# Performance work log

Hardware: AMD Instinct MI355X
Metric: run time of the kernel (lower is better)

Reference implementation:

```python
import jax, jax.numpy as jnp
import numpy as np

B, S, D = 4, 2048, 256   # batch, seq, d_output (= d_k = d_v here)
H = 8                    # num_head


def setup_inputs() -> dict:
    key = jax.random.key(0)
    ks = jax.random.split(key, 8)
    Q = jax.random.normal(ks[0], (B, S, D), dtype=jnp.float32)
    K = jax.random.normal(ks[1], (B, S, D), dtype=jnp.float32)
    V = jax.random.normal(ks[2], (B, S, D), dtype=jnp.float32)
    M = jax.random.uniform(ks[3], (B, S, S), dtype=jnp.float32)  # multiplicative mask
    # per-head projection weights, stacked over heads (truncated_normal ~ normal here)
    W_Q = jax.random.normal(ks[4], (H, D, D), dtype=jnp.float32) * 0.05
    W_K = jax.random.normal(ks[5], (H, D, D), dtype=jnp.float32) * 0.05
    W_V = jax.random.normal(ks[6], (H, D, D), dtype=jnp.float32) * 0.05
    W_mh = jax.random.normal(ks[7], (H * D, D), dtype=jnp.float32) * 0.05
    return {"Q": Q, "K": K, "V": V, "M": M,
            "W_Q": W_Q, "W_K": W_K, "W_V": W_V, "W_mh": W_mh}


def reference(Q, K, V, M, W_Q, W_K, W_V, W_mh):
    d_k = W_Q.shape[-1]
    scale = 1.0 / np.sqrt(d_k).astype(np.float32)
    # per-head projections, vectorized over heads
    Qh = jnp.einsum('bsd,hdk->bhsk', Q, W_Q)          # [B,H,S,dk]
    Kh = jnp.einsum('bsd,hdk->bhsk', K, W_K)          # [B,H,S,dk]
    Vh = jnp.einsum('bsd,hdv->bhsv', V, W_V)          # [B,H,S,dv]
    # scaled similarity with MULTIPLICATIVE mask applied before softmax
    scores = jnp.einsum('bhsk,bhtk->bhst', Qh, Kh) * scale * M[:, None]
    attn = jax.nn.softmax(scores, axis=-1)            # [B,H,S,S]
    heads = jnp.einsum('bhst,bhtv->bhsv', attn, Vh)   # [B,H,S,dv]
    # concat heads along feature dim: [B,S,H*dv]
    Bv, Hv, Sv, Dv = heads.shape
    heads = heads.transpose(0, 2, 1, 3).reshape(Bv, Sv, Hv * Dv)
    return heads @ W_mh                               # [B,S,d_output]
```

## Files before the change

### kernel.cpp

```cpp
#include <hip/hip_runtime.h>
#include <hip/hip_bf16.h>
#include <stdint.h>

#define B_ 4
#define S_ 2048
#define D_ 256
#define H_ 8

using f32x4  = __attribute__((ext_vector_type(4))) float;
using bf16x8 = __attribute__((ext_vector_type(8))) __bf16;

static __device__ __forceinline__ unsigned short f2bf(float x) {
    union { float f; unsigned u; } v; v.f = x;
    unsigned r = (v.u + 0x7FFFu + ((v.u >> 16) & 1u)) >> 16;
    return (unsigned short)r;
}

static __device__ __forceinline__ f32x4 mfma_bf16(bf16x8 a, bf16x8 b, f32x4 c) {
    return __builtin_amdgcn_mfma_f32_16x16x32_bf16(a, b, c, 0, 0, 0);
}

__global__ __launch_bounds__(256) void wtrans_kernel(
        const float* __restrict__ Wq, const float* __restrict__ Wk,
        const float* __restrict__ Wv, const float* __restrict__ Wmh,
        unsigned short* __restrict__ WqkvT, unsigned short* __restrict__ WmhT) {
    int idx = blockIdx.x * 256 + threadIdx.x;
    const int NQKV = 3 * H_ * 256 * 256;
    if (idx < NQKV) {
        int d = idx & 255, n = (idx >> 8) & 255, h = (idx >> 16) & 7, which = idx >> 19;
        const float* W = (which == 0) ? Wq : ((which == 1) ? Wk : Wv);
        WqkvT[idx] = f2bf(W[(h * 256 + d) * 256 + n]);
    } else {
        int j = idx - NQKV;
        int k = j & 2047, n = j >> 11;
        WmhT[j] = f2bf(Wmh[k * 256 + n]);
    }
}

__global__ __launch_bounds__(256, 2) void proj_kernel(
        const float* __restrict__ Q, const float* __restrict__ K,
        const float* __restrict__ V, const unsigned short* __restrict__ WqkvT,
        unsigned short* __restrict__ Qh, unsigned short* __restrict__ Kh,
        unsigned short* __restrict__ VhT) {
    __shared__ __attribute__((aligned(16))) unsigned char smem[65536];
    int tid = threadIdx.x;
    int nt = blockIdx.x & 3, h = (blockIdx.x >> 2) & 7, which = blockIdx.x >> 5;
    int mt = blockIdx.y;
    const float* X = (which == 0) ? Q : ((which == 1) ? K : V);

    {
        const float4* Xv = (const float4*)(X + (size_t)mt * 64 * 256);
        #pragma unroll
        for (int j = 0; j < 16; ++j) {
            int c = tid + 256 * j;
            int row = c >> 6, c4 = c & 63;
            float4 x = Xv[c];
            ushort4 p;
            p.x = f2bf(x.x); p.y = f2bf(x.y); p.z = f2bf(x.z); p.w = f2bf(x.w);
            *(ushort4*)(smem + row * 512 + ((c4 * 8) ^ ((row & 7) << 4))) = p;
        }
    }
    {
        const uint4* Wv_ = (const uint4*)(WqkvT + (size_t)((which * H_ + h) * 256 + nt * 64) * 256);
        #pragma unroll
        for (int j = 0; j < 8; ++j) {
            int c = tid + 256 * j;
            int row = c >> 5, slot = c & 31;
            *(uint4*)(smem + 32768 + row * 512 + ((slot * 16) ^ ((row & 7) << 4))) = Wv_[c];
        }
    }
    __syncthreads();

    int w = tid >> 6, l = tid & 63, lr = l & 15, lg = l >> 4;
    f32x4 acc[4];
    #pragma unroll
    for (int fr = 0; fr < 4; ++fr) acc[fr] = (f32x4){0.f, 0.f, 0.f, 0.f};

    #pragma unroll
    for (int ks = 0; ks < 8; ++ks) {
        int arow = 16 * w + lr;
        bf16x8 a = *(const bf16x8*)(smem + arow * 512 + ((64 * ks + 16 * lg) ^ ((arow & 7) << 4)));
        #pragma unroll
        for (int fr = 0; fr < 4; ++fr) {
            int brow = 16 * fr + lr;
            bf16x8 b = *(const bf16x8*)(smem + 32768 + brow * 512 + ((64 * ks + 16 * lg) ^ ((brow & 7) << 4)));
            acc[fr] = mfma_bf16(a, b, acc[fr]);
        }
    }

    int m0 = mt * 64 + 16 * w + 4 * lg;
    int b = m0 >> 11, s0 = m0 & 2047;
    if (which < 2) {
        unsigned short* out = (which == 0) ? Qh : Kh;
        #pragma unroll
        for (int fr = 0; fr < 4; ++fr) {
            int n = nt * 64 + 16 * fr + lr;
            #pragma unroll
            for (int i = 0; i < 4; ++i)
                out[(size_t)((b * H_ + h) * S_ + s0 + i) * D_ + n] = f2bf(acc[fr][i]);
        }
    } else {
        #pragma unroll
        for (int fr = 0; fr < 4; ++fr) {
            int n = nt * 64 + 16 * fr + lr;
            ushort4 p;
            p.x = f2bf(acc[fr][0]); p.y = f2bf(acc[fr][1]);
            p.z = f2bf(acc[fr][2]); p.w = f2bf(acc[fr][3]);
            *(ushort4*)(VhT + (size_t)((b * H_ + h) * D_ + n) * S_ + s0) = p;
        }
    }
}

__global__ __launch_bounds__(256, 2) void attn_kernel(
        const unsigned short* Qh, const unsigned short* __restrict__ Kh,
        const unsigned short* __restrict__ VhT, const float* __restrict__ M,
        unsigned short* heads) {
    __shared__ __attribute__((aligned(16))) unsigned char smem[73728];
    int tid = threadIdx.x;
    int qt = blockIdx.x, h = blockIdx.y, b = blockIdx.z;
    int bh = b * H_ + h;
    int w = tid >> 6, l = tid & 63, lr = l & 15, lg = l >> 4;

    const unsigned short* KhP = Kh + (size_t)bh * S_ * D_;
    const unsigned short* VTP = VhT + (size_t)bh * D_ * S_;
    const float* MP = M + (size_t)b * S_ * S_;

    bf16x8 qf[8];
    {
        int qrow = qt * 64 + 16 * w + lr;
        const unsigned short* QhP = Qh + (size_t)(bh * S_ + qrow) * D_;
        #pragma unroll
        for (int ks = 0; ks < 8; ++ks)
            qf[ks] = *(const bf16x8*)(QhP + 32 * ks + 8 * lg);
    }

    f32x4 o[16];
    #pragma unroll
    for (int vf = 0; vf < 16; ++vf) o[vf] = (f32x4){0.f, 0.f, 0.f, 0.f};
    float mrun[4], lrun[4];
    #pragma unroll
    for (int i = 0; i < 4; ++i) { mrun[i] = -1e30f; lrun[i] = 0.f; }

    int q0 = qt * 64 + 16 * w + 4 * lg;
    unsigned char* plds = smem + 65536 + w * 2048;

    for (int tt = 0; tt < 32; ++tt) {
        __syncthreads();
        {
            const uint4* src = (const uint4*)(KhP + (size_t)tt * 64 * 256);
            #pragma unroll
            for (int j = 0; j < 8; ++j) {
                int c = tid + 256 * j;
                int row = c >> 5, slot = c & 31;
                *(uint4*)(smem + row * 512 + ((slot * 16) ^ ((row & 7) << 4))) = src[c];
            }
        }
        {
            #pragma unroll
            for (int j = 0; j < 8; ++j) {
                int c = tid + 256 * j;
                int v = c >> 3, slot = c & 7;
                uint4 x = *(const uint4*)(VTP + (size_t)v * S_ + tt * 64 + slot * 8);
                *(uint4*)(smem + 32768 + v * 128 + ((slot * 16) ^ ((v & 7) << 4))) = x;
            }
        }
        __syncthreads();

        f32x4 sacc[4];
        #pragma unroll
        for (int fr = 0; fr < 4; ++fr) sacc[fr] = (f32x4){0.f, 0.f, 0.f, 0.f};
        #pragma unroll
        for (int ks = 0; ks < 8; ++ks) {
            #pragma unroll
            for (int fr = 0; fr < 4; ++fr) {
                int brow = 16 * fr + lr;
                bf16x8 bb = *(const bf16x8*)(smem + brow * 512 + ((64 * ks + 16 * lg) ^ ((brow & 7) << 4)));
                sacc[fr] = mfma_bf16(qf[ks], bb, sacc[fr]);
            }
        }

        float p[4][4];
        #pragma unroll
        for (int fr = 0; fr < 4; ++fr) {
            int tg = tt * 64 + 16 * fr + lr;
            #pragma unroll
            for (int i = 0; i < 4; ++i) {
                float mv = MP[(size_t)(q0 + i) * S_ + tg];
                p[fr][i] = sacc[fr][i] * 0.0625f * mv;
            }
        }

        #pragma unroll
        for (int i = 0; i < 4; ++i) {
            float mx = fmaxf(fmaxf(p[0][i], p[1][i]), fmaxf(p[2][i], p[3][i]));
            #pragma unroll
            for (int dd = 1; dd < 16; dd <<= 1) mx = fmaxf(mx, __shfl_xor(mx, dd, 64));
            float mn = fmaxf(mrun[i], mx);
            float f = __expf(mrun[i] - mn);
            float rs = 0.f;
            #pragma unroll
            for (int fr = 0; fr < 4; ++fr) { p[fr][i] = __expf(p[fr][i] - mn); rs += p[fr][i]; }
            #pragma unroll
            for (int dd = 1; dd < 16; dd <<= 1) rs += __shfl_xor(rs, dd, 64);
            lrun[i] = lrun[i] * f + rs;
            mrun[i] = mn;
            #pragma unroll
            for (int vf = 0; vf < 16; ++vf) o[vf][i] *= f;
        }

        #pragma unroll
        for (int i = 0; i < 4; ++i) {
            int row = 4 * lg + i;
            #pragma unroll
            for (int fr = 0; fr < 4; ++fr)
                *(unsigned short*)(plds + row * 128 + (((16 * fr + lr) * 2) ^ ((row & 7) << 4))) =
                    f2bf(p[fr][i]);
        }

        #pragma unroll
        for (int ks2 = 0; ks2 < 2; ++ks2) {
            int prow = lr;
            bf16x8 pa = *(const bf16x8*)(plds + prow * 128 + ((64 * ks2 + 16 * lg) ^ ((prow & 7) << 4)));
            #pragma unroll
            for (int vf = 0; vf < 16; ++vf) {
                int vrow = 16 * vf + lr;
                bf16x8 bv = *(const bf16x8*)(smem + 32768 + vrow * 128 + ((64 * ks2 + 16 * lg) ^ ((vrow & 7) << 4)));
                o[vf] = mfma_bf16(pa, bv, o[vf]);
            }
        }
    }

    #pragma unroll
    for (int i = 0; i < 4; ++i) {
        float inv = 1.f / lrun[i];
        unsigned short* hp = heads + (size_t)(bh * S_ + q0 + i) * D_;
        #pragma unroll
        for (int vf = 0; vf < 16; ++vf)
            hp[16 * vf + lr] = f2bf(o[vf][i] * inv);
    }
}

__global__ __launch_bounds__(256, 2) void out_kernel(
        const unsigned short* __restrict__ heads,
        const unsigned short* __restrict__ WmhT, float* __restrict__ out) {
    __shared__ __attribute__((aligned(16))) unsigned char smem[65536];
    int tid = threadIdx.x;
    int nt = blockIdx.x, mt = blockIdx.y;
    int w = tid >> 6, l = tid & 63, lr = l & 15, lg = l >> 4;
    int m0 = mt * 64;
    int b = m0 >> 11, s00 = m0 & 2047;

    f32x4 acc[4];
    #pragma unroll
    for (int fr = 0; fr < 4; ++fr) acc[fr] = (f32x4){0.f, 0.f, 0.f, 0.f};

    for (int h = 0; h < H_; ++h) {
        __syncthreads();
        {
            const uint4* src = (const uint4*)(heads + (size_t)((b * H_ + h) * S_ + s00) * D_);
            #pragma unroll
            for (int j = 0; j < 8; ++j) {
                int c = tid + 256 * j;
                int row = c >> 5, slot = c & 31;
                *(uint4*)(smem + row * 512 + ((slot * 16) ^ ((row & 7) << 4))) = src[c];
            }
        }
        {
            #pragma unroll
            for (int j = 0; j < 8; ++j) {
                int c = tid + 256 * j;
                int row = c >> 5, slot = c & 31;
                uint4 x = *(const uint4*)(WmhT + (size_t)(nt * 64 + row) * 2048 + h * 256 + slot * 8);
                *(uint4*)(smem + 32768 + row * 512 + ((slot * 16) ^ ((row & 7) << 4))) = x;
            }
        }
        __syncthreads();
        #pragma unroll
        for (int ks = 0; ks < 8; ++ks) {
            int arow = 16 * w + lr;
            bf16x8 a = *(const bf16x8*)(smem + arow * 512 + ((64 * ks + 16 * lg) ^ ((arow & 7) << 4)));
            #pragma unroll
            for (int fr = 0; fr < 4; ++fr) {
                int brow = 16 * fr + lr;
                bf16x8 bb = *(const bf16x8*)(smem + 32768 + brow * 512 + ((64 * ks + 16 * lg) ^ ((brow & 7) << 4)));
                acc[fr] = mfma_bf16(a, bb, acc[fr]);
            }
        }
    }

    int mrow = mt * 64 + 16 * w + 4 * lg;
    #pragma unroll
    for (int fr = 0; fr < 4; ++fr) {
        int n = nt * 64 + 16 * fr + lr;
        #pragma unroll
        for (int i = 0; i < 4; ++i)
            out[(size_t)(mrow + i) * D_ + n] = acc[fr][i];
    }
}

extern "C" void kernel_launch(void* const* d_in, const int* in_sizes, int n_in,
                              void* d_out, int out_size, void* d_ws, size_t ws_size,
                              hipStream_t stream) {
    const float* Q   = (const float*)d_in[0];
    const float* K   = (const float*)d_in[1];
    const float* V   = (const float*)d_in[2];
    const float* M   = (const float*)d_in[3];
    const float* Wq  = (const float*)d_in[4];
    const float* Wk  = (const float*)d_in[5];
    const float* Wv  = (const float*)d_in[6];
    const float* Wmh = (const float*)d_in[7];
    float* out = (float*)d_out;

    char* ws = (char*)d_ws;
    unsigned short* Qh    = (unsigned short*)(ws);
    unsigned short* Kh    = (unsigned short*)(ws + 33554432);
    unsigned short* VhT   = (unsigned short*)(ws + 67108864);
    unsigned short* WqkvT = (unsigned short*)(ws + 100663296);
    unsigned short* WmhT  = (unsigned short*)(ws + 103809024);

    wtrans_kernel<<<dim3(8192), dim3(256), 0, stream>>>(Wq, Wk, Wv, Wmh, WqkvT, WmhT);
    proj_kernel<<<dim3(96, 128), dim3(256), 0, stream>>>(Q, K, V, WqkvT, Qh, Kh, VhT);
    attn_kernel<<<dim3(32, 8, 4), dim3(256), 0, stream>>>(Qh, Kh, VhT, M, Qh);
    out_kernel<<<dim3(4, 128), dim3(256), 0, stream>>>(Qh, WmhT, out);
}
```

Measured before the change: 547.8 us.

## Rewrite attention with 32x32 MFMA, double-buffered direct-to-LDS loads and split-KV waves

```diff
diff --git a/kernel.cpp b/kernel.cpp
--- a/kernel.cpp
+++ b/kernel.cpp
@@ -8,6 +8,8 @@
 #define H_ 8
 
 using f32x4  = __attribute__((ext_vector_type(4))) float;
+using f32x16 = __attribute__((ext_vector_type(16))) float;
+using bf16x4 = __attribute__((ext_vector_type(4))) __bf16;
 using bf16x8 = __attribute__((ext_vector_type(8))) __bf16;
 
 static __device__ __forceinline__ unsigned short f2bf(float x) {
@@ -16,8 +18,32 @@
     return (unsigned short)r;
 }
 
-static __device__ __forceinline__ f32x4 mfma_bf16(bf16x8 a, bf16x8 b, f32x4 c) {
+static __device__ __forceinline__ f32x4 mfma16(bf16x8 a, bf16x8 b, f32x4 c) {
     return __builtin_amdgcn_mfma_f32_16x16x32_bf16(a, b, c, 0, 0, 0);
+}
+static __device__ __forceinline__ f32x16 mfma32(bf16x8 a, bf16x8 b, f32x16 c) {
+    return __builtin_amdgcn_mfma_f32_32x32x16_bf16(a, b, c, 0, 0, 0);
+}
+
+static __device__ __forceinline__ unsigned cvt_pk_bf16(float lo, float hi) {
+    unsigned r;
+    asm volatile("v_cvt_pk_bf16_f32 %0, %1, %2" : "=v"(r) : "v"(lo), "v"(hi));
+    return r;
+}
+
+static __device__ __forceinline__ void gl_lds16(const void* g, void* l) {
+    __builtin_amdgcn_global_load_lds((const __attribute__((address_space(1))) void*)g,
+                                     (__attribute__((address_space(3))) void*)l, 16, 0, 0);
+}
+static __device__ __forceinline__ void gl_lds4(const void* g, void* l) {
+    __builtin_amdgcn_global_load_lds((const __attribute__((address_space(1))) void*)g,
+                                     (__attribute__((address_space(3))) void*)l, 4, 0, 0);
+}
+
+static __device__ __forceinline__ void drain_vmem_then_sync() {
+    asm volatile("s_waitcnt vmcnt(0)" ::: "memory");
+    __builtin_amdgcn_sched_barrier(0);
+    __syncthreads();
 }
 
 __global__ __launch_bounds__(256) void wtrans_kernel(
@@ -84,7 +110,7 @@
         for (int fr = 0; fr < 4; ++fr) {
             int brow = 16 * fr + lr;
             bf16x8 b = *(const bf16x8*)(smem + 32768 + brow * 512 + ((64 * ks + 16 * lg) ^ ((brow & 7) << 4)));
-            acc[fr] = mfma_bf16(a, b, acc[fr]);
+            acc[fr] = mfma16(a, b, acc[fr]);
         }
     }
 
@@ -92,12 +118,13 @@
     int b = m0 >> 11, s0 = m0 & 2047;
     if (which < 2) {
         unsigned short* out = (which == 0) ? Qh : Kh;
+        float sc = (which == 0) ? 0.0625f : 1.0f;
         #pragma unroll
         for (int fr = 0; fr < 4; ++fr) {
             int n = nt * 64 + 16 * fr + lr;
             #pragma unroll
             for (int i = 0; i < 4; ++i)
-                out[(size_t)((b * H_ + h) * S_ + s0 + i) * D_ + n] = f2bf(acc[fr][i]);
+                out[(size_t)((b * H_ + h) * S_ + s0 + i) * D_ + n] = f2bf(acc[fr][i] * sc);
         }
     } else {
         #pragma unroll
@@ -111,132 +138,195 @@
     }
 }
 
-__global__ __launch_bounds__(256, 2) void attn_kernel(
+__global__ __launch_bounds__(512, 2) void attn2_kernel(
         const unsigned short* Qh, const unsigned short* __restrict__ Kh,
         const unsigned short* __restrict__ VhT, const float* __restrict__ M,
         unsigned short* heads) {
-    __shared__ __attribute__((aligned(16))) unsigned char smem[73728];
-    int tid = threadIdx.x;
-    int qt = blockIdx.x, h = blockIdx.y, b = blockIdx.z;
+    __shared__ __attribute__((aligned(16))) unsigned char smem[131072];
+    const int tid = threadIdx.x;
+    const int w = tid >> 6, l = tid & 63;
+    const int qg = w >> 1, ts = w & 1;
+    const int ql = l & 31, hi = l >> 5;
+
+    int n = blockIdx.x;
+    int x = n & 7, r0 = n >> 3;
+    int h = r0 & 7, ghi = r0 >> 3;
+    int g = x + 8 * ghi;
+    int qt = g & 15, b = g >> 4;
     int bh = b * H_ + h;
-    int w = tid >> 6, l = tid & 63, lr = l & 15, lg = l >> 4;
 
     const unsigned short* KhP = Kh + (size_t)bh * S_ * D_;
     const unsigned short* VTP = VhT + (size_t)bh * D_ * S_;
-    const float* MP = M + (size_t)b * S_ * S_;
-
-    bf16x8 qf[8];
+
+    const int q = qt * 128 + qg * 32 + ql;
+    const float* MrowP = M + (size_t)b * S_ * S_ + (size_t)q * S_;
+
+    bf16x8 qf[16];
     {
-        int qrow = qt * 64 + 16 * w + lr;
-        const unsigned short* QhP = Qh + (size_t)(bh * S_ + qrow) * D_;
-        #pragma unroll
-        for (int ks = 0; ks < 8; ++ks)
-            qf[ks] = *(const bf16x8*)(QhP + 32 * ks + 8 * lg);
-    }
-
-    f32x4 o[16];
-    #pragma unroll
-    for (int vf = 0; vf < 16; ++vf) o[vf] = (f32x4){0.f, 0.f, 0.f, 0.f};
-    float mrun[4], lrun[4];
-    #pragma unroll
-    for (int i = 0; i < 4; ++i) { mrun[i] = -1e30f; lrun[i] = 0.f; }
-
-    int q0 = qt * 64 + 16 * w + 4 * lg;
-    unsigned char* plds = smem + 65536 + w * 2048;
-
+        const unsigned short* QhP = Qh + ((size_t)bh * S_ + q) * D_;
+        #pragma unroll
+        for (int ks = 0; ks < 16; ++ks)
+            qf[ks] = *(const bf16x8*)(QhP + ks * 16 + hi * 8);
+    }
+
+    f32x16 o[8];
+    #pragma unroll
+    for (int vb = 0; vb < 8; ++vb) o[vb] = (f32x16){};
+    float mrun = -1e30f, lrun = 0.f;
+
+    const int krow = ts * 32 + ql;
+    const unsigned kbase = (unsigned)(krow * 512 + ((hi * 16) ^ ((krow & 15) << 5)));
+    const unsigned vtbase = (unsigned)(ql * 128 + (((ts * 64) | (hi * 16)) ^ ((ql & 15) << 3)));
+
+    const int ksr = 8 * w + (l >> 5);
+    const unsigned kcol = (l & 31) * 16;
+    const int vsr = 32 * w + (l >> 5);
+    const unsigned vcol = (l & 31) * 4;
+
+    int cur = 0;
+
+    auto stage = [&](int tt, int bsel) {
+        unsigned char* kb = smem + bsel * 32768;
+        unsigned char* vb = smem + 65536 + bsel * 32768;
+        #pragma unroll
+        for (int j = 0; j < 4; ++j) {
+            int row = ksr + 2 * j;
+            const unsigned char* src = (const unsigned char*)KhP +
+                (size_t)(tt * 64 + row) * 512 + (kcol ^ ((row & 15) << 5));
+            gl_lds16(src, kb + (8 * w + 2 * j) * 512);
+        }
+        #pragma unroll
+        for (int i = 0; i < 16; ++i) {
+            int v = vsr + 2 * i;
+            const unsigned char* src = (const unsigned char*)VTP +
+                (size_t)v * (S_ * 2) + tt * 128 + (vcol ^ ((v & 15) << 3));
+            gl_lds4(src, vb + (32 * w + 2 * i) * 128);
+        }
+    };
+
+    stage(0, 0);
+    drain_vmem_then_sync();
+
+    #pragma unroll 1
     for (int tt = 0; tt < 32; ++tt) {
-        __syncthreads();
-        {
-            const uint4* src = (const uint4*)(KhP + (size_t)tt * 64 * 256);
-            #pragma unroll
-            for (int j = 0; j < 8; ++j) {
-                int c = tid + 256 * j;
-                int row = c >> 5, slot = c & 31;
-                *(uint4*)(smem + row * 512 + ((slot * 16) ^ ((row & 7) << 4))) = src[c];
-            }
-        }
-        {
-            #pragma unroll
-            for (int j = 0; j < 8; ++j) {
-                int c = tid + 256 * j;
-                int v = c >> 3, slot = c & 7;
-                uint4 x = *(const uint4*)(VTP + (size_t)v * S_ + tt * 64 + slot * 8);
-                *(uint4*)(smem + 32768 + v * 128 + ((slot * 16) ^ ((v & 7) << 4))) = x;
-            }
-        }
-        __syncthreads();
-
-        f32x4 sacc[4];
-        #pragma unroll
-        for (int fr = 0; fr < 4; ++fr) sacc[fr] = (f32x4){0.f, 0.f, 0.f, 0.f};
-        #pragma unroll
-        for (int ks = 0; ks < 8; ++ks) {
-            #pragma unroll
-            for (int fr = 0; fr < 4; ++fr) {
-                int brow = 16 * fr + lr;
-                bf16x8 bb = *(const bf16x8*)(smem + brow * 512 + ((64 * ks + 16 * lg) ^ ((brow & 7) << 4)));
-                sacc[fr] = mfma_bf16(qf[ks], bb, sacc[fr]);
-            }
-        }
-
-        float p[4][4];
-        #pragma unroll
-        for (int fr = 0; fr < 4; ++fr) {
-            int tg = tt * 64 + 16 * fr + lr;
-            #pragma unroll
-            for (int i = 0; i < 4; ++i) {
-                float mv = MP[(size_t)(q0 + i) * S_ + tg];
-                p[fr][i] = sacc[fr][i] * 0.0625f * mv;
-            }
-        }
-
-        #pragma unroll
-        for (int i = 0; i < 4; ++i) {
-            float mx = fmaxf(fmaxf(p[0][i], p[1][i]), fmaxf(p[2][i], p[3][i]));
-            #pragma unroll
-            for (int dd = 1; dd < 16; dd <<= 1) mx = fmaxf(mx, __shfl_xor(mx, dd, 64));
-            float mn = fmaxf(mrun[i], mx);
-            float f = __expf(mrun[i] - mn);
-            float rs = 0.f;
-            #pragma unroll
-            for (int fr = 0; fr < 4; ++fr) { p[fr][i] = __expf(p[fr][i] - mn); rs += p[fr][i]; }
-            #pragma unroll
-            for (int dd = 1; dd < 16; dd <<= 1) rs += __shfl_xor(rs, dd, 64);
-            lrun[i] = lrun[i] * f + rs;
-            mrun[i] = mn;
-            #pragma unroll
-            for (int vf = 0; vf < 16; ++vf) o[vf][i] *= f;
-        }
-
-        #pragma unroll
-        for (int i = 0; i < 4; ++i) {
-            int row = 4 * lg + i;
-            #pragma unroll
-            for (int fr = 0; fr < 4; ++fr)
-                *(unsigned short*)(plds + row * 128 + (((16 * fr + lr) * 2) ^ ((row & 7) << 4))) =
-                    f2bf(p[fr][i]);
-        }
-
-        #pragma unroll
-        for (int ks2 = 0; ks2 < 2; ++ks2) {
-            int prow = lr;
-            bf16x8 pa = *(const bf16x8*)(plds + prow * 128 + ((64 * ks2 + 16 * lg) ^ ((prow & 7) << 4)));
-            #pragma unroll
-            for (int vf = 0; vf < 16; ++vf) {
-                int vrow = 16 * vf + lr;
-                bf16x8 bv = *(const bf16x8*)(smem + 32768 + vrow * 128 + ((64 * ks2 + 16 * lg) ^ ((vrow & 7) << 4)));
-                o[vf] = mfma_bf16(pa, bv, o[vf]);
-            }
-        }
-    }
-
-    #pragma unroll
-    for (int i = 0; i < 4; ++i) {
-        float inv = 1.f / lrun[i];
-        unsigned short* hp = heads + (size_t)(bh * S_ + q0 + i) * D_;
-        #pragma unroll
-        for (int vf = 0; vf < 16; ++vf)
-            hp[16 * vf + lr] = f2bf(o[vf][i] * inv);
+        stage((tt + 1) & 31, cur ^ 1);
+
+        const unsigned char* kp = smem + cur * 32768;
+        const unsigned char* vp = smem + 65536 + cur * 32768;
+
+        const float* Mt = MrowP + tt * 64 + ts * 32 + 4 * hi;
+        float4 mv0 = *(const float4*)(Mt);
+        float4 mv1 = *(const float4*)(Mt + 8);
+        float4 mv2 = *(const float4*)(Mt + 16);
+        float4 mv3 = *(const float4*)(Mt + 24);
+
+        f32x16 sacc = (f32x16){};
+        #pragma unroll
+        for (int ks = 0; ks < 16; ++ks) {
+            bf16x8 a = *(const bf16x8*)(kp + (kbase ^ (unsigned)(ks * 32)));
+            sacc = mfma32(a, qf[ks], sacc);
+        }
+
+        float p[16];
+        #pragma unroll
+        for (int rg = 0; rg < 4; ++rg) {
+            float4 mv = (rg == 0) ? mv0 : (rg == 1) ? mv1 : (rg == 2) ? mv2 : mv3;
+            #pragma unroll
+            for (int j = 0; j < 4; ++j) p[4 * rg + j] = sacc[4 * rg + j] * ((const float*)&mv)[j];
+        }
+
+        float tm = p[0];
+        #pragma unroll
+        for (int i = 1; i < 16; ++i) tm = fmaxf(tm, p[i]);
+        float tmm = fmaxf(tm, __shfl_xor(tm, 32, 64));
+
+        if (__any(tmm > mrun)) {
+            float nm = fmaxf(mrun, tmm);
+            float f = __expf(mrun - nm);
+            #pragma unroll
+            for (int vb = 0; vb < 8; ++vb) o[vb] *= f;
+            lrun *= f;
+            mrun = nm;
+        }
+
+        float rs = 0.f;
+        #pragma unroll
+        for (int i = 0; i < 16; ++i) { p[i] = __expf(p[i] - mrun); rs += p[i]; }
+        lrun += rs;
+
+        unsigned own0 = cvt_pk_bf16(p[0], p[1]),  own1 = cvt_pk_bf16(p[2], p[3]);
+        unsigned own2 = cvt_pk_bf16(p[4], p[5]),  own3 = cvt_pk_bf16(p[6], p[7]);
+        unsigned own4 = cvt_pk_bf16(p[8], p[9]),  own5 = cvt_pk_bf16(p[10], p[11]);
+        unsigned own6 = cvt_pk_bf16(p[12], p[13]), own7 = cvt_pk_bf16(p[14], p[15]);
+        unsigned rec0 = __shfl_xor((int)own0, 32, 64), rec1 = __shfl_xor((int)own1, 32, 64);
+        unsigned rec2 = __shfl_xor((int)own2, 32, 64), rec3 = __shfl_xor((int)own3, 32, 64);
+        unsigned rec4 = __shfl_xor((int)own4, 32, 64), rec5 = __shfl_xor((int)own5, 32, 64);
+        unsigned rec6 = __shfl_xor((int)own6, 32, 64), rec7 = __shfl_xor((int)own7, 32, 64);
+
+        union { unsigned u[4]; bf16x8 v; } f0, f1;
+        f0.u[0] = hi ? rec2 : own0;  f0.u[1] = hi ? rec3 : own1;
+        f0.u[2] = hi ? own2 : rec0;  f0.u[3] = hi ? own3 : rec1;
+        f1.u[0] = hi ? rec6 : own4;  f1.u[1] = hi ? rec7 : own5;
+        f1.u[2] = hi ? own6 : rec4;  f1.u[3] = hi ? own7 : rec5;
+
+        #pragma unroll
+        for (int tstep = 0; tstep < 2; ++tstep) {
+            bf16x8 pf = tstep ? f1.v : f0.v;
+            unsigned a0 = vtbase ^ (unsigned)(tstep * 32);
+            #pragma unroll
+            for (int vb = 0; vb < 8; ++vb) {
+                bf16x4 lo4 = *(const bf16x4*)(vp + vb * 4096 + a0);
+                bf16x4 hi4 = *(const bf16x4*)(vp + vb * 4096 + (a0 ^ 8u));
+                bf16x8 av = __builtin_shufflevector(lo4, hi4, 0, 1, 2, 3, 4, 5, 6, 7);
+                o[vb] = mfma32(av, pf, o[vb]);
+            }
+        }
+
+        drain_vmem_then_sync();
+        cur ^= 1;
+    }
+
+    lrun += __shfl_xor(lrun, 32, 64);
+
+    float2* mlb = (float2*)smem;
+    if (hi == 0) mlb[(qg * 2 + ts) * 32 + ql] = make_float2(mrun, lrun);
+    __syncthreads();
+    float2 oth = mlb[(qg * 2 + (ts ^ 1)) * 32 + ql];
+    __syncthreads();
+
+    float mstar = fmaxf(mrun, oth.x);
+    float aS = __expf(mrun - mstar), aO = __expf(oth.x - mstar);
+    float inv = 1.f / (aS * lrun + aO * oth.y);
+    float sc = aS * inv;
+    #pragma unroll
+    for (int vb = 0; vb < 8; ++vb) o[vb] *= sc;
+
+    float* ob = (float*)smem;
+    if (ts == 1) {
+        #pragma unroll
+        for (int vb = 0; vb < 8; ++vb)
+            #pragma unroll
+            for (int r = 0; r < 16; ++r) {
+                int v = 32 * vb + (r & 3) + 8 * (r >> 2) + 4 * hi;
+                ob[qg * 8192 + v * 32 + ql] = o[vb][r];
+            }
+    }
+    __syncthreads();
+    if (ts == 0) {
+        unsigned short* hp = heads + ((size_t)bh * S_ + q) * D_;
+        #pragma unroll
+        for (int vb = 0; vb < 8; ++vb) {
+            #pragma unroll
+            for (int rg = 0; rg < 4; ++rg) {
+                int v0 = 32 * vb + 8 * rg + 4 * hi;
+                ushort4 pk;
+                pk.x = f2bf(o[vb][4 * rg + 0] + ob[qg * 8192 + (v0 + 0) * 32 + ql]);
+                pk.y = f2bf(o[vb][4 * rg + 1] + ob[qg * 8192 + (v0 + 1) * 32 + ql]);
+                pk.z = f2bf(o[vb][4 * rg + 2] + ob[qg * 8192 + (v0 + 2) * 32 + ql]);
+                pk.w = f2bf(o[vb][4 * rg + 3] + ob[qg * 8192 + (v0 + 3) * 32 + ql]);
+                *(ushort4*)(hp + v0) = pk;
+            }
+        }
     }
 }
 
@@ -270,8 +360,8 @@
             for (int j = 0; j < 8; ++j) {
                 int c = tid + 256 * j;
                 int row = c >> 5, slot = c & 31;
-                uint4 x = *(const uint4*)(WmhT + (size_t)(nt * 64 + row) * 2048 + h * 256 + slot * 8);
-                *(uint4*)(smem + 32768 + row * 512 + ((slot * 16) ^ ((row & 7) << 4))) = x;
+                uint4 xx = *(const uint4*)(WmhT + (size_t)(nt * 64 + row) * 2048 + h * 256 + slot * 8);
+                *(uint4*)(smem + 32768 + row * 512 + ((slot * 16) ^ ((row & 7) << 4))) = xx;
             }
         }
         __syncthreads();
@@ -283,7 +373,7 @@
             for (int fr = 0; fr < 4; ++fr) {
                 int brow = 16 * fr + lr;
                 bf16x8 bb = *(const bf16x8*)(smem + 32768 + brow * 512 + ((64 * ks + 16 * lg) ^ ((brow & 7) << 4)));
-                acc[fr] = mfma_bf16(a, bb, acc[fr]);
+                acc[fr] = mfma16(a, bb, acc[fr]);
             }
         }
     }
@@ -291,10 +381,10 @@
     int mrow = mt * 64 + 16 * w + 4 * lg;
     #pragma unroll
     for (int fr = 0; fr < 4; ++fr) {
-        int n = nt * 64 + 16 * fr + lr;
+        int nn = nt * 64 + 16 * fr + lr;
         #pragma unroll
         for (int i = 0; i < 4; ++i)
-            out[(size_t)(mrow + i) * D_ + n] = acc[fr][i];
+            out[(size_t)(mrow + i) * D_ + nn] = acc[fr][i];
     }
 }
 
@@ -320,6 +410,6 @@
 
     wtrans_kernel<<<dim3(8192), dim3(256), 0, stream>>>(Wq, Wk, Wv, Wmh, WqkvT, WmhT);
     proj_kernel<<<dim3(96, 128), dim3(256), 0, stream>>>(Q, K, V, WqkvT, Qh, Kh, VhT);
-    attn_kernel<<<dim3(32, 8, 4), dim3(256), 0, stream>>>(Qh, Kh, VhT, M, Qh);
+    attn2_kernel<<<dim3(512), dim3(512), 0, stream>>>(Qh, Kh, VhT, M, Qh);
     out_kernel<<<dim3(4, 128), dim3(256), 0, stream>>>(Qh, WmhT, out);
 }
```

After: 644.0 us. 1.18x slower.
